# Optimization experiments

Measured on AMD Instinct MI355X. Metric: run time of the kernel, lower is better.

Reference implementation:

```python
import jax, jax.numpy as jnp
import numpy as np

G = 32          # latent grid size per axis
CIN = 3         # in_channels
C = 64          # fno_hidden_channels
M = 8           # half modes per axis (n_modes=16 -> 8)
L = 4           # fno_n_layers
LIFT = 256      # fno_lifting_channels
PROJ = 256      # projection_channels
N_IN = G ** 3
N_OUT = 16384
E = 262144      # total neighbor pairs from radius search


def _gelu(x):
    return jax.nn.gelu(x, approximate=False)  # matches torch F.gelu


def _spectral_conv(x, wr, wi):
    # x: (1, Ci, G, G, G); wr/wi: (4, Ci, Co, M, M, M) -- 4 frequency corners
    xf = jnp.fft.rfftn(x, axes=(2, 3, 4), norm='forward')
    w = wr + 1j * wi
    of = jnp.zeros((x.shape[0], wr.shape[2]) + xf.shape[2:], dtype=xf.dtype)
    corners = [(slice(0, M), slice(0, M)), (slice(0, M), slice(-M, None)),
               (slice(-M, None), slice(0, M)), (slice(-M, None), slice(-M, None))]
    for k, (s1, s2) in enumerate(corners):
        of = of.at[:, :, s1, s2, :M].set(
            jnp.einsum('bixyz,ioxyz->boxyz', xf[:, :, s1, s2, :M], w[k]))
    return jnp.fft.irfftn(of, s=x.shape[2:4] + x.shape[4:], axes=(2, 3, 4), norm='forward')


def setup_inputs() -> dict:
    key = jax.random.key(0)
    ks = jax.random.split(key, 32)
    s = 0.02
    inp = {}
    inp['in_p'] = jax.random.uniform(ks[0], (G, G, G, 3), jnp.float32)
    inp['out_p'] = jax.random.uniform(ks[1], (N_OUT, 3), jnp.float32)
    inp['f'] = jax.random.normal(ks[2], (G, G, G, CIN), jnp.float32)
    inp['nb_in_idx'] = jax.random.randint(ks[3], (E,), 0, N_IN)
    inp['nb_seg'] = jnp.sort(jax.random.randint(ks[4], (E,), 0, N_OUT))
    # FNO lifting (2-layer pointwise MLP): (in+coord)=6 -> LIFT -> C
    inp['lift_w1'] = jax.random.normal(ks[5], (LIFT, CIN + 3)) * s
    inp['lift_b1'] = jnp.zeros((LIFT,), jnp.float32)
    inp['lift_w2'] = jax.random.normal(ks[6], (C, LIFT)) * s
    inp['lift_b2'] = jnp.zeros((C,), jnp.float32)
    # Spectral conv weights: (L, 4 corners, Ci, Co, M, M, M)
    sc = 1.0 / (C * C)
    inp['spec_wr'] = jax.random.normal(ks[7], (L, 4, C, C, M, M, M)) * sc
    inp['spec_wi'] = jax.random.normal(ks[8], (L, 4, C, C, M, M, M)) * sc
    inp['skip_w'] = jax.random.normal(ks[9], (L, C, C)) * s
    inp['skip_b'] = jnp.zeros((L, C), jnp.float32)
    # GNO kernel MLP: [6, 512, 256, 64]
    inp['gno_w1'] = jax.random.normal(ks[10], (512, 6)) * s
    inp['gno_b1'] = jnp.zeros((512,), jnp.float32)
    inp['gno_w2'] = jax.random.normal(ks[11], (256, 512)) * s
    inp['gno_b2'] = jnp.zeros((256,), jnp.float32)
    inp['gno_w3'] = jax.random.normal(ks[12], (C, 256)) * s
    inp['gno_b3'] = jnp.zeros((C,), jnp.float32)
    # projection MLP: C -> PROJ -> out_channels(=1)
    inp['proj_w1'] = jax.random.normal(ks[13], (PROJ, C)) * s
    inp['proj_b1'] = jnp.zeros((PROJ,), jnp.float32)
    inp['proj_w2'] = jax.random.normal(ks[14], (1, PROJ)) * s
    inp['proj_b2'] = jnp.zeros((1,), jnp.float32)
    return inp


def reference(in_p, out_p, f, nb_in_idx, nb_seg,
              lift_w1, lift_b1, lift_w2, lift_b2,
              spec_wr, spec_wi, skip_w, skip_b,
              gno_w1, gno_b1, gno_w2, gno_b2, gno_w3, gno_b3,
              proj_w1, proj_b1, proj_w2, proj_b2):
    # ---- latent_embedding: FNO over the grid ----
    x = jnp.concatenate([f, in_p], axis=-1).transpose(3, 0, 1, 2)[None]  # (1,6,G,G,G)
    x = _gelu(jnp.einsum('bixyz,oi->boxyz', x, lift_w1) + lift_b1[None, :, None, None, None])
    x = jnp.einsum('bixyz,oi->boxyz', x, lift_w2) + lift_b2[None, :, None, None, None]
    for l in range(L):
        x = (_spectral_conv(x, spec_wr[l], spec_wi[l])
             + jnp.einsum('bixyz,oi->boxyz', x, skip_w[l])
             + skip_b[l][None, :, None, None, None])
        if l < L - 1:
            x = _gelu(x)
    latent = x[0].transpose(1, 2, 3, 0).reshape(N_IN, C)  # (n_in, C)
    # ---- integrate_latent: gather -> kernel MLP -> scale by f_y -> segment mean ----
    y = in_p.reshape(N_IN, 3)
    feats = jnp.concatenate([y[nb_in_idx], out_p[nb_seg]], axis=-1)  # (E, 6)
    h = _gelu(feats @ gno_w1.T + gno_b1)
    h = _gelu(h @ gno_w2.T + gno_b2)
    kern = h @ gno_w3.T + gno_b3                     # (E, C)
    contrib = kern * latent[nb_in_idx]               # linear transform: k(x,y)*f(y)
    ssum = jax.ops.segment_sum(contrib, nb_seg, num_segments=N_OUT)
    cnt = jax.ops.segment_sum(jnp.ones((E, 1), contrib.dtype), nb_seg, num_segments=N_OUT)
    out = ssum / jnp.maximum(cnt, 1.0)               # (n_out, C)
    # ---- projection MLP ----
    h = _gelu(out @ proj_w1.T + proj_b1)
    return h @ proj_w2.T + proj_b2                   # (n_out, 1)
```

## Files before the change

kernel.cpp:

```cpp
#include <hip/hip_runtime.h>

typedef unsigned short u16;
typedef float f32x4 __attribute__((ext_vector_type(4)));
typedef _Float16 f16x8 __attribute__((ext_vector_type(8)));
typedef u16 us8 __attribute__((ext_vector_type(8)));

#define PI2f 6.283185307179586f
#define NE_TOT 262144
#define N_IN_TOT 32768
#define N_OUT_TOT 16384

__device__ __forceinline__ float gelu_f(float x){
  float t  = 0.70710678118654752f * x;
  float t2 = t * t;
  float p = t*(1.1283791670955126f + t2*(-0.37612638903183754f + t2*(0.11283791670955126f
            + t2*(-0.026866170645131253f + t2*(0.005223977625442188f + t2*(-0.0008548327023450853f))))));
  return 0.5f * x * (1.0f + p);
}
__device__ __forceinline__ float gelu_s(float x){
  float t  = 0.70710678118654752f * x;
  float t2 = t * t;
  float p = t*(1.1283791670955126f + t2*(-0.37612638903183754f + t2*(0.11283791670955126f
            + t2*(-0.026866170645131253f))));
  return 0.5f * x * (1.0f + p);
}

__device__ __forceinline__ u16 f2h(float x){
  _Float16 h = (_Float16)x;
  return __builtin_bit_cast(u16, h);
}
__device__ __forceinline__ float h2f(u16 h){
  return (float)__builtin_bit_cast(_Float16, h);
}

__global__ __launch_bounds__(256) void k_pack(const float* w2, const float* w3, u16* B2p, u16* B3p){
  int tid = blockIdx.x*256 + threadIdx.x;
  if (tid < 16*16*64*8){
    int e = tid & 7, l = (tid>>3)&63, nt = (tid>>9)&15, ks = tid>>13;
    int n = nt*16 + (l&15);
    int k = ks*32 + (l>>4)*8 + e;
    B2p[tid] = f2h(w2[n*512 + k]);
  }
  int t2 = tid - 16*16*64*8;
  if (t2 >= 0 && t2 < 8*4*64*8){
    int e = t2 & 7, l = (t2>>3)&63, nt = (t2>>9)&3, ks = t2>>11;
    int n = nt*16 + (l&15);
    int k = ks*32 + (l>>4)*8 + e;
    B3p[t2] = f2h(w3[n*256 + k]);
  }
}

__global__ __launch_bounds__(256) void k_lift_s1(const float* f, const float* in_p,
      const float* w1, const float* b1, const float* w2, const float* b2, float* v, float* T1){
  extern __shared__ char smem[];
  float* h   = (float*)smem;
  float* w2t = h + 64*256;
  float* xf  = w2t + 256*65;
  float* vt2 = h;
  float* twc = xf;
  float* tws = xf + 256;
  int t = threadIdx.x;
  int p0 = blockIdx.x * 64;
  for (int idx = t; idx < 64*6; idx += 256){
    int e = idx/6, k = idx - e*6;
    xf[e*8 + k] = (k < 3) ? f[(p0+e)*3 + k] : in_p[(p0+e)*3 + (k-3)];
  }
  for (int i4 = t; i4 < 4096; i4 += 256){
    const float4 wv = ((const float4*)w2)[i4];
    int c = i4 >> 6, u = (i4 & 63)*4;
    w2t[(u+0)*65 + c] = wv.x;
    w2t[(u+1)*65 + c] = wv.y;
    w2t[(u+2)*65 + c] = wv.z;
    w2t[(u+3)*65 + c] = wv.w;
  }
  __syncthreads();
  {
    int u = t;
    float wr[6];
    #pragma unroll
    for (int k = 0; k < 6; ++k) wr[k] = w1[u*6 + k];
    float bb = b1[u];
    for (int e = 0; e < 64; ++e){
      float s = bb;
      #pragma unroll
      for (int k = 0; k < 6; ++k) s += wr[k]*xf[e*8+k];
      h[e*256 + u] = gelu_f(s);
    }
  }
  __syncthreads();
  {
    int kz = t >> 5, z = t & 31;
    float sv, cv;
    sincosf(PI2f * (float)(kz*z) / 32.0f, &sv, &cv);
    twc[t] = cv; tws[t] = sv;
  }
  int c = t & 63, zg = t >> 6;
  float acc[16];
  {
    #pragma unroll
    for (int i=0;i<16;++i) acc[i]=0.f;
    for (int u4 = 0; u4 < 64; ++u4){
      float wv0 = w2t[(u4*4+0)*65 + c];
      float wv1 = w2t[(u4*4+1)*65 + c];
      float wv2 = w2t[(u4*4+2)*65 + c];
      float wv3 = w2t[(u4*4+3)*65 + c];
      #pragma unroll
      for (int ee = 0; ee < 16; ++ee){
        const float4 hv = *(const float4*)&h[(zg*16+ee)*256 + u4*4];
        acc[ee] += wv0*hv.x + wv1*hv.y + wv2*hv.z + wv3*hv.w;
      }
    }
  }
  __syncthreads();
  {
    float bb = b2[c];
    #pragma unroll
    for (int ee = 0; ee < 16; ++ee){
      float val = acc[ee] + bb;
      int pl = zg*16 + ee;
      v[(size_t)(p0 + pl)*64 + c] = val;
      vt2[pl*64 + c] = val;
    }
  }
  __syncthreads();
  const float sc = 1.0f/32768.0f;
  int kzg = t >> 6;
  int kza = kzg, kzb = kzg + 4;
  float2* o = (float2*)T1;
  #pragma unroll
  for (int xyl = 0; xyl < 2; ++xyl){
    const float* vt = vt2 + xyl*2048;
    int xy = blockIdx.x*2 + xyl;
    float re0=0,im0=0,re1=0,im1=0;
    for (int z = 0; z < 32; ++z){
      float vv = vt[z*64 + c];
      re0 += vv * twc[kza*32+z]; im0 -= vv * tws[kza*32+z];
      re1 += vv * twc[kzb*32+z]; im1 -= vv * tws[kzb*32+z];
    }
    o[(xy*8 + kza)*64 + c] = make_float2(re0*sc, im0*sc);
    o[(xy*8 + kzb)*64 + c] = make_float2(re1*sc, im1*sc);
  }
}

__global__ __launch_bounds__(256) void k_s2(const float* T1, float* T2){
  __shared__ float t1s[2048];
  __shared__ float twc[512], tws[512];
  int t = threadIdx.x;
  int x = blockIdx.x >> 4, kz = (blockIdx.x >> 1) & 7, ch = blockIdx.x & 1;
  for (int i = t; i < 512; i += 256){
    int kyi = i >> 5, y = i & 31;
    int ky = (kyi < 8) ? kyi : kyi + 16;
    float sv, cv; sincosf(PI2f * (float)(ky*y) / 32.0f, &sv, &cv);
    twc[i]=cv; tws[i]=sv;
  }
  for (int i4 = t; i4 < 512; i4 += 256){
    int y = i4 >> 4, q4 = i4 & 15;
    ((float4*)t1s)[i4] = *((const float4*)&T1[((size_t)((x*32+y)*8 + kz))*128 + ch*64] + q4);
  }
  __syncthreads();
  int cl = t & 31, g = t >> 5;
  float ar[2], ai[2];
  ar[0]=0;ar[1]=0;ai[0]=0;ai[1]=0;
  for (int y = 0; y < 32; ++y){
    float tr = t1s[(y*32+cl)*2], ti = t1s[(y*32+cl)*2+1];
    #pragma unroll
    for (int kk = 0; kk < 2; ++kk){
      int kyi = g + kk*8;
      float cc = twc[kyi*32+y], ss = tws[kyi*32+y];
      ar[kk] += tr*cc + ti*ss;
      ai[kk] += ti*cc - tr*ss;
    }
  }
  float2* o = (float2*)T2;
  int c = ch*32 + cl;
  #pragma unroll
  for (int kk = 0; kk < 2; ++kk){
    int kyi = g + kk*8;
    o[((x*16 + kyi)*8 + kz)*64 + c] = make_float2(ar[kk], ai[kk]);
  }
}

__global__ __launch_bounds__(256) void k_s3(const float* T2, float* F){
  __shared__ float t2s[1024];
  __shared__ float twc[512], tws[512];
  int t = threadIdx.x;
  int kyi = blockIdx.x >> 5, kz = (blockIdx.x >> 2) & 7, cq = blockIdx.x & 3;
  for (int i = t; i < 512; i += 256){
    int kxi = i >> 5, x = i & 31;
    int kx = (kxi < 8) ? kxi : kxi + 16;
    float sv, cv; sincosf(PI2f * (float)(kx*x) / 32.0f, &sv, &cv);
    twc[i]=cv; tws[i]=sv;
  }
  if (t < 256){
    int i4 = t;
    int x = i4 >> 3, q4 = i4 & 7;
    ((float4*)t2s)[i4] = *((const float4*)&T2[((size_t)((x*16+kyi)*8 + kz))*128 + cq*32] + q4);
  }
  __syncthreads();
  int cl = t & 15, kxi = t >> 4;
  float ar = 0.f, ai = 0.f;
  for (int x = 0; x < 32; ++x){
    float tr = t2s[(x*16+cl)*2], ti = t2s[(x*16+cl)*2+1];
    float cc = twc[kxi*32+x], ss = tws[kxi*32+x];
    ar += tr*cc + ti*ss;
    ai += ti*cc - tr*ss;
  }
  float2* o = (float2*)F;
  int c = cq*16 + cl;
  o[((kxi*16 + kyi)*8 + kz)*64 + c] = make_float2(ar, ai);
}

__global__ __launch_bounds__(256) void k_s4(const float* F, const float* wr, const float* wi, float* OFp){
  __shared__ float FT[16*65*2];
  int t = threadIdx.x;
  int bid = blockIdx.x;
  int oh = bid & 7, ic = (bid>>3)&3, mx = (bid>>6)&7, corner = bid>>9;
  int kxi = (corner>>1)*8 + mx;
  int kyb = (corner&1)*8;
  for (int idx = t; idx < 2048; idx += 256){
    int m = idx >> 5, w = idx & 31;
    int cl = w >> 1, part = w & 1;
    int my = m >> 3, kz = m & 7;
    FT[(cl*65 + m)*2 + part] = F[((size_t)((kxi*16 + kyb + my)*8 + kz))*128 + ic*32 + w];
  }
  __syncthreads();
  int m = t & 63, og = t >> 6;
  int my = m >> 3, kz = m & 7;
  float accr[2], acci[2];
  accr[0]=0;accr[1]=0;acci[0]=0;acci[1]=0;
  #pragma unroll 4
  for (int i = 0; i < 16; ++i){
    float fr = FT[(i*65+m)*2], fi = FT[(i*65+m)*2+1];
    size_t rowbase = ((size_t)(corner*64 + ic*16 + i))*64;
    #pragma unroll
    for (int oo = 0; oo < 2; ++oo){
      int o = oh*8 + og*2 + oo;
      size_t widx = (rowbase + o)*512 + mx*64 + m;
      float wrv = wr[widx], wiv = wi[widx];
      accr[oo] += wrv*fr - wiv*fi;
      acci[oo] += wrv*fi + wiv*fr;
    }
  }
  float2* o2 = (float2*)OFp;
  size_t obase = (size_t)ic*131072 + ((size_t)((kxi*16 + kyb + my)*8 + kz))*64;
  #pragma unroll
  for (int oo = 0; oo < 2; ++oo){
    int o = oh*8 + og*2 + oo;
    o2[obase + o] = make_float2(accr[oo], acci[oo]);
  }
}

__global__ __launch_bounds__(256) void k_s5(const float* OFp, float* G1){
  __shared__ float OFs[512];
  __shared__ float twc[512], tws[512];
  int t = threadIdx.x;
  int kyi = blockIdx.x >> 5, kz = (blockIdx.x >> 2) & 7, oq = blockIdx.x & 3;
  for (int i = t; i < 512; i += 256){
    int kxi = i >> 5, x = i & 31;
    int kx = (kxi < 8) ? kxi : kxi + 16;
    float sv, cv; sincosf(PI2f * (float)(kx*x) / 32.0f, &sv, &cv);
    twc[i]=cv; tws[i]=sv;
  }
  if (t < 128){
    int i4 = t;
    int kx = i4 >> 3, w4 = i4 & 7;
    float4 s = {0.f,0.f,0.f,0.f};
    #pragma unroll
    for (int p = 0; p < 4; ++p){
      const float4 vv = *((const float4*)&OFp[(size_t)p*262144 + ((size_t)((kx*16+kyi)*8+kz))*128 + oq*32] + w4);
      s.x += vv.x; s.y += vv.y; s.z += vv.z; s.w += vv.w;
    }
    ((float4*)OFs)[i4] = s;
  }
  __syncthreads();
  int ol = t & 15, g = t >> 4;
  float ar[2], ai[2];
  ar[0]=0;ar[1]=0;ai[0]=0;ai[1]=0;
  for (int kxi = 0; kxi < 16; ++kxi){
    float orr = OFs[(kxi*16+ol)*2], oii = OFs[(kxi*16+ol)*2+1];
    #pragma unroll
    for (int xx = 0; xx < 2; ++xx){
      int x = g + xx*16;
      float cc = twc[kxi*32+x], ss = tws[kxi*32+x];
      ar[xx] += orr*cc - oii*ss;
      ai[xx] += orr*ss + oii*cc;
    }
  }
  float2* o2 = (float2*)G1;
  int o = oq*16 + ol;
  #pragma unroll
  for (int xx = 0; xx < 2; ++xx){
    int x = g + xx*16;
    o2[((x*16 + kyi)*8 + kz)*64 + o] = make_float2(ar[xx], ai[xx]);
  }
}

__global__ __launch_bounds__(256) void k_s6(const float* G1, float* G2){
  __shared__ float g1s[1024];
  __shared__ float twc[512], tws[512];
  int t = threadIdx.x;
  int x = blockIdx.x >> 4, kz = (blockIdx.x >> 1) & 7, oh = blockIdx.x & 1;
  for (int i = t; i < 512; i += 256){
    int kyi = i >> 5, y = i & 31;
    int ky = (kyi < 8) ? kyi : kyi + 16;
    float sv, cv; sincosf(PI2f * (float)(ky*y) / 32.0f, &sv, &cv);
    twc[i]=cv; tws[i]=sv;
  }
  if (t < 256){
    int i4 = t;
    int kyi = i4 >> 4, w4 = i4 & 15;
    ((float4*)g1s)[i4] = *((const float4*)&G1[((size_t)((x*16+kyi)*8+kz))*128 + oh*64] + w4);
  }
  __syncthreads();
  int ol = t & 31, g = t >> 5;
  float ar[4], ai[4];
  #pragma unroll
  for (int i=0;i<4;++i){ar[i]=0;ai[i]=0;}
  for (int kyi = 0; kyi < 16; ++kyi){
    float gr = g1s[(kyi*32+ol)*2], gi = g1s[(kyi*32+ol)*2+1];
    #pragma unroll
    for (int yy = 0; yy < 4; ++yy){
      int y = g + yy*8;
      float cc = twc[kyi*32+y], ss = tws[kyi*32+y];
      ar[yy] += gr*cc - gi*ss;
      ai[yy] += gr*ss + gi*cc;
    }
  }
  float2* o2 = (float2*)G2;
  int o = oh*32 + ol;
  #pragma unroll
  for (int yy = 0; yy < 4; ++yy){
    int y = g + yy*8;
    o2[((x*32 + y)*8 + kz)*64 + o] = make_float2(ar[yy], ai[yy]);
  }
}

__global__ __launch_bounds__(256) void k_s7s1(const float* G2, const float* vin,
      const float* skw, const float* skb, float* vout, float* T1){
  __shared__ float g2s[1024];
  __shared__ float vt[2048];
  __shared__ float wT[64*65];
  __shared__ float twc[256], tws[256];
  __shared__ float sb[64];
  int t = threadIdx.x;
  int xy = blockIdx.x;
  {
    int kz = t >> 5, z = t & 31;
    float sv, cv; sincosf(PI2f * (float)(kz*z) / 32.0f, &sv, &cv);
    twc[t]=cv; tws[t]=sv;
  }
  { int i4 = t; if (i4 < 256) ((float4*)g2s)[i4] = ((const float4*)(G2 + (size_t)xy*1024))[i4]; }
  for (int i4 = t; i4 < 512; i4 += 256)
    ((float4*)vt)[i4] = ((const float4*)(vin + (size_t)xy*2048))[i4];
  for (int i4 = t; i4 < 1024; i4 += 256){
    const float4 wv = ((const float4*)skw)[i4];
    int cc = i4 >> 4, ii = (i4 & 15)*4;
    wT[(ii+0)*65 + cc] = wv.x;
    wT[(ii+1)*65 + cc] = wv.y;
    wT[(ii+2)*65 + cc] = wv.z;
    wT[(ii+3)*65 + cc] = wv.w;
  }
  if (t < 64) sb[t] = skb[t];
  __syncthreads();
  int c = t & 63, zg = t >> 6;
  float accz[8];
  #pragma unroll
  for (int zz=0; zz<8; ++zz){
    int z = zg*8 + zz;
    float s = g2s[c*2];
    #pragma unroll
    for (int kz=1; kz<8; ++kz){
      float gr = g2s[(kz*64+c)*2], gi = g2s[(kz*64+c)*2+1];
      s += 2.0f*(gr*twc[kz*32+z] - gi*tws[kz*32+z]);
    }
    accz[zz] = s + sb[c];
  }
  for (int i4 = 0; i4 < 16; ++i4){
    float w0 = wT[(i4*4+0)*65 + c];
    float w1v = wT[(i4*4+1)*65 + c];
    float w2v = wT[(i4*4+2)*65 + c];
    float w3v = wT[(i4*4+3)*65 + c];
    #pragma unroll
    for (int zz=0; zz<8; ++zz){
      const float4 vv = *(const float4*)&vt[(zg*8+zz)*64 + i4*4];
      accz[zz] += w0*vv.x + w1v*vv.y + w2v*vv.z + w3v*vv.w;
    }
  }
  __syncthreads();
  #pragma unroll
  for (int zz=0; zz<8; ++zz){
    float s = gelu_f(accz[zz]);
    int z = zg*8 + zz;
    vout[(size_t)(xy*32 + z)*64 + c] = s;
    vt[z*64 + c] = s;
  }
  __syncthreads();
  {
    const float sc = 1.0f/32768.0f;
    int kzg = t >> 6;
    int kza = kzg, kzb = kzg + 4;
    float re0=0,im0=0,re1=0,im1=0;
    for (int z = 0; z < 32; ++z){
      float vv = vt[z*64 + c];
      re0 += vv * twc[kza*32+z]; im0 -= vv * tws[kza*32+z];
      re1 += vv * twc[kzb*32+z]; im1 -= vv * tws[kzb*32+z];
    }
    float2* o = (float2*)T1;
    o[(xy*8 + kza)*64 + c] = make_float2(re0*sc, im0*sc);
    o[(xy*8 + kzb)*64 + c] = make_float2(re1*sc, im1*sc);
  }
}

__global__ __launch_bounds__(256) void k_s7(const float* G2, const float* vin,
      const float* skw, const float* skb, float* vout, int dogelu){
  __shared__ float g2s[1024];
  __shared__ float vt[2048];
  __shared__ float wT[64*65];
  __shared__ float twc[256], tws[256];
  __shared__ float sb[64];
  int t = threadIdx.x;
  int xy = blockIdx.x;
  {
    int kz = t >> 5, z = t & 31;
    float sv, cv; sincosf(PI2f * (float)(kz*z) / 32.0f, &sv, &cv);
    twc[t]=cv; tws[t]=sv;
  }
  { int i4 = t; if (i4 < 256) ((float4*)g2s)[i4] = ((const float4*)(G2 + (size_t)xy*1024))[i4]; }
  for (int i4 = t; i4 < 512; i4 += 256)
    ((float4*)vt)[i4] = ((const float4*)(vin + (size_t)xy*2048))[i4];
  for (int i4 = t; i4 < 1024; i4 += 256){
    const float4 wv = ((const float4*)skw)[i4];
    int cc = i4 >> 4, ii = (i4 & 15)*4;
    wT[(ii+0)*65 + cc] = wv.x;
    wT[(ii+1)*65 + cc] = wv.y;
    wT[(ii+2)*65 + cc] = wv.z;
    wT[(ii+3)*65 + cc] = wv.w;
  }
  if (t < 64) sb[t] = skb[t];
  __syncthreads();
  int c = t & 63, zg = t >> 6;
  float accz[8];
  #pragma unroll
  for (int zz=0; zz<8; ++zz){
    int z = zg*8 + zz;
    float s = g2s[c*2];
    #pragma unroll
    for (int kz=1; kz<8; ++kz){
      float gr = g2s[(kz*64+c)*2], gi = g2s[(kz*64+c)*2+1];
      s += 2.0f*(gr*twc[kz*32+z] - gi*tws[kz*32+z]);
    }
    accz[zz] = s + sb[c];
  }
  for (int i4 = 0; i4 < 16; ++i4){
    float w0 = wT[(i4*4+0)*65 + c];
    float w1v = wT[(i4*4+1)*65 + c];
    float w2v = wT[(i4*4+2)*65 + c];
    float w3v = wT[(i4*4+3)*65 + c];
    #pragma unroll
    for (int zz=0; zz<8; ++zz){
      const float4 vv = *(const float4*)&vt[(zg*8+zz)*64 + i4*4];
      accz[zz] += w0*vv.x + w1v*vv.y + w2v*vv.z + w3v*vv.w;
    }
  }
  #pragma unroll
  for (int zz=0; zz<8; ++zz){
    float s = accz[zz];
    if (dogelu) s = gelu_f(s);
    vout[(size_t)(xy*32 + zg*8 + zz)*64 + c] = s;
  }
}

__global__ __launch_bounds__(256, 4) void k_gno(
    const int* nb_i, const int* nb_j, const float* in_p, const float* out_p,
    const float* w1, const float* b1, const float* b2g, const float* b3g,
    const u16* B2p, const u16* B3p, const float* latent, float* contrib){
  extern __shared__ char smem[];
  u16*   h1c   = (u16*)smem;
  u16*   h2s   = (u16*)smem;
  float* feats = (float*)(smem + 32768);
  float* sb2   = feats + 512;
  float* sb3   = sb2 + 256;
  int*   idxE  = (int*)(sb3 + 64);
  int t = threadIdx.x;
  int e0 = blockIdx.x * 64;
  if (t < 64){
    int gi = nb_i[e0 + t];
    int gj = nb_j[e0 + t];
    idxE[t] = gi;
    feats[t*8+0] = in_p[gi*3+0];
    feats[t*8+1] = in_p[gi*3+1];
    feats[t*8+2] = in_p[gi*3+2];
    feats[t*8+3] = out_p[gj*3+0];
    feats[t*8+4] = out_p[gj*3+1];
    feats[t*8+5] = out_p[gj*3+2];
    sb3[t] = b3g[t];
  }
  sb2[t] = b2g[t];
  int l = t & 63, w = t >> 6;
  int up = t & 63;
  int eg = t >> 6;
  f32x4 acc[4][4];
  #pragma unroll
  for (int m=0;m<4;++m)
    #pragma unroll
    for (int n=0;n<4;++n) acc[m][n] = (f32x4){0.f,0.f,0.f,0.f};
  __syncthreads();

  for (int chunk = 0; chunk < 4; ++chunk){
    int u0 = chunk*128 + up*2;
    float wa[6], wb[6];
    #pragma unroll
    for (int k=0;k<6;++k){ wa[k]=w1[u0*6+k]; wb[k]=w1[u0*6+6+k]; }
    float ba = b1[u0], bb = b1[u0+1];
    #pragma unroll 4
    for (int n = 0; n < 16; ++n){
      int e = eg*16 + n;
      const float4 fa = *(const float4*)&feats[e*8];
      const float4 fb = *(const float4*)&feats[e*8+4];
      float s0 = ba + wa[0]*fa.x + wa[1]*fa.y + wa[2]*fa.z + wa[3]*fa.w + wa[4]*fb.x + wa[5]*fb.y;
      float s1 = bb + wb[0]*fa.x + wb[1]*fa.y + wb[2]*fa.z + wb[3]*fa.w + wb[4]*fb.x + wb[5]*fb.y;
      unsigned lo = f2h(gelu_s(s0));
      unsigned hi = f2h(gelu_s(s1));
      int bofs = (e*256 + up*4) ^ ((e&7)<<4);
      *(unsigned*)((char*)h1c + bofs) = lo | (hi<<16);
    }
    __syncthreads();
    #pragma unroll
    for (int ks2 = 0; ks2 < 4; ++ks2){
      int gk = chunk*4 + ks2;
      f16x8 af[4];
      #pragma unroll
      for (int m=0;m<4;++m){
        int row = m*16 + (l&15);
        int bofs = (row*256 + ks2*64 + (l>>4)*16) ^ ((row&7)<<4);
        af[m] = __builtin_bit_cast(f16x8, *(const us8*)((const char*)h1c + bofs));
      }
      f16x8 bq[4];
      #pragma unroll
      for (int nt=0;nt<4;++nt){
        int ntg = w*4 + nt;
        bq[nt] = __builtin_bit_cast(f16x8, *(const us8*)(B2p + ((gk*16 + ntg)*64 + l)*8));
      }
      #pragma unroll
      for (int m=0;m<4;++m)
        #pragma unroll
        for (int nt=0;nt<4;++nt)
          acc[m][nt] = __builtin_amdgcn_mfma_f32_16x16x32_f16(af[m], bq[nt], acc[m][nt], 0, 0, 0);
    }
    __syncthreads();
  }

  #pragma unroll
  for (int m=0;m<4;++m){
    #pragma unroll
    for (int nt=0;nt<4;++nt){
      #pragma unroll
      for (int r=0;r<4;++r){
        int row = m*16 + (l>>4)*4 + r;
        int n = w*64 + nt*16 + (l&15);
        float vv = gelu_s(acc[m][nt][r] + sb2[n]);
        int bofs = (row*512 + n*2) ^ ((row&7)<<4);
        *(u16*)((char*)h2s + bofs) = f2h(vv);
      }
    }
  }
  __syncthreads();
  f32x4 a3[4];
  #pragma unroll
  for (int m=0;m<4;++m) a3[m] = (f32x4){0.f,0.f,0.f,0.f};
  #pragma unroll
  for (int ks = 0; ks < 8; ++ks){
    f16x8 bq3 = __builtin_bit_cast(f16x8, *(const us8*)(B3p + ((ks*4 + w)*64 + l)*8));
    #pragma unroll
    for (int m=0;m<4;++m){
      int row = m*16 + (l&15);
      int bofs = (row*512 + ks*64 + (l>>4)*16) ^ ((row&7)<<4);
      f16x8 am = __builtin_bit_cast(f16x8, *(const us8*)((const char*)h2s + bofs));
      a3[m] = __builtin_amdgcn_mfma_f32_16x16x32_f16(am, bq3, a3[m], 0, 0, 0);
    }
  }
  {
    int q = l >> 4;
    int c = w*16 + (l&15);
    float b3c = sb3[c];
    #pragma unroll
    for (int m=0;m<4;++m){
      #pragma unroll
      for (int r=0;r<4;++r){
        int e = m*16 + q*4 + r;
        float kern = a3[m][r] + b3c;
        contrib[((size_t)(e0+e))*64 + c] = kern * latent[(size_t)idxE[e]*64 + c];
      }
    }
  }
}

__global__ __launch_bounds__(256) void k_segmean(const int* seg, const float* contrib, float* outseg){
  int t = threadIdx.x;
  int j = blockIdx.x*4 + (t>>6);
  int lane = t & 63;
  int lo = 0, hi = NE_TOT;
  while (lo < hi){ int mid = (lo+hi)>>1; if (seg[mid] < j) lo = mid+1; else hi = mid; }
  int s0 = lo;
  hi = NE_TOT;
  while (lo < hi){ int mid = (lo+hi)>>1; if (seg[mid] < j+1) lo = mid+1; else hi = mid; }
  int s1 = lo;
  float s = 0.f;
  for (int e = s0; e < s1; ++e) s += contrib[(size_t)e*64 + lane];
  outseg[(size_t)j*64 + lane] = s / fmaxf((float)(s1 - s0), 1.0f);
}

__global__ __launch_bounds__(256) void k_proj(const float* outseg, const float* w1, const float* b1,
                                              const float* w2, const float* b2, float* out){
  __shared__ float rows[64*68];
  __shared__ float w1s[256*68];
  __shared__ float w2s[256];
  __shared__ float b1s[256];
  __shared__ float red[256];
  int t = threadIdx.x;
  int r0 = blockIdx.x * 64;
  for (int idx = t; idx < 4096; idx += 256){
    int e = idx >> 6, c = idx & 63;
    rows[e*68 + c] = outseg[(size_t)(r0+e)*64 + c];
  }
  for (int idx = t; idx < 16384; idx += 256){
    int u = idx >> 6, c = idx & 63;
    w1s[u*68 + c] = w1[idx];
  }
  w2s[t] = w2[t];
  b1s[t] = b1[t];
  __syncthreads();
  int e = t >> 2, q = t & 3;
  float fsum = 0.f;
  for (int uu = 0; uu < 64; ++uu){
    int u = uu*4 + q;
    float pre = b1s[u];
    #pragma unroll
    for (int c4 = 0; c4 < 16; ++c4){
      const float4 a = *(const float4*)&w1s[u*68 + c4*4];
      const float4 r = *(const float4*)&rows[e*68 + c4*4];
      pre += a.x*r.x + a.y*r.y + a.z*r.z + a.w*r.w;
    }
    fsum += w2s[u] * gelu_f(pre);
  }
  red[t] = fsum;
  __syncthreads();
  if (t < 64){
    out[r0 + t] = red[t*4] + red[t*4+1] + red[t*4+2] + red[t*4+3] + b2[0];
  }
}

extern "C" void kernel_launch(void* const* d_in, const int* in_sizes, int n_in,
                              void* d_out, int out_size, void* d_ws, size_t ws_size,
                              hipStream_t stream){
  const float* in_p  = (const float*)d_in[0];
  const float* out_p = (const float*)d_in[1];
  const float* f     = (const float*)d_in[2];
  const int*   nb_i  = (const int*)d_in[3];
  const int*   nb_j  = (const int*)d_in[4];
  const float* lw1   = (const float*)d_in[5];
  const float* lb1   = (const float*)d_in[6];
  const float* lw2   = (const float*)d_in[7];
  const float* lb2   = (const float*)d_in[8];
  const float* swr   = (const float*)d_in[9];
  const float* swi   = (const float*)d_in[10];
  const float* skw   = (const float*)d_in[11];
  const float* skb   = (const float*)d_in[12];
  const float* gw1   = (const float*)d_in[13];
  const float* gb1   = (const float*)d_in[14];
  const float* gw2   = (const float*)d_in[15];
  const float* gb2   = (const float*)d_in[16];
  const float* gw3   = (const float*)d_in[17];
  const float* gb3   = (const float*)d_in[18];
  const float* pw1   = (const float*)d_in[19];
  const float* pb1   = (const float*)d_in[20];
  const float* pw2   = (const float*)d_in[21];
  const float* pb2   = (const float*)d_in[22];
  float* out = (float*)d_out;

  char* ws = (char*)d_ws;
  size_t off = 0;
  auto alloc = [&](size_t bytes)->void*{ void* p = ws + off; off += (bytes + 255) & ~(size_t)255; return p; };
  float* va      = (float*)alloc((size_t)N_IN_TOT*64*4);
  float* vb      = (float*)alloc((size_t)N_IN_TOT*64*4);
  float* T1      = (float*)alloc((size_t)32*32*8*64*2*4);
  float* T2      = (float*)alloc((size_t)32*16*8*64*2*4);
  float* Fq      = (float*)alloc((size_t)16*16*8*64*2*4);
  float* OFp     = (float*)alloc((size_t)4*16*16*8*64*2*4);
  float* G1      = (float*)alloc((size_t)32*16*8*64*2*4);
  float* G2      = (float*)alloc((size_t)32*32*8*64*2*4);
  u16*   B2p     = (u16*)alloc((size_t)16*16*64*8*2);
  u16*   B3p     = (u16*)alloc((size_t)8*4*64*8*2);
  float* contrib = (float*)alloc((size_t)NE_TOT*64*4);
  float* outseg  = (float*)alloc((size_t)N_OUT_TOT*64*4);


  k_pack<<<576, 256, 0, stream>>>(gw2, gw3, B2p, B3p);
  k_lift_s1<<<512, 256, 134144, stream>>>(f, in_p, lw1, lb1, lw2, lb2, va, T1);

  float* vin = va; float* vout = vb;
  for (int layer = 0; layer < 4; ++layer){
    k_s2<<<512, 256, 0, stream>>>(T1, T2);
    k_s3<<<512, 256, 0, stream>>>(T2, Fq);
    k_s4<<<1024, 256, 0, stream>>>(Fq, swr + (size_t)layer*4*64*64*512, swi + (size_t)layer*4*64*64*512, OFp);
    k_s5<<<512, 256, 0, stream>>>(OFp, G1);
    k_s6<<<512, 256, 0, stream>>>(G1, G2);
    if (layer < 3)
      k_s7s1<<<1024, 256, 0, stream>>>(G2, vin, skw + layer*64*64, skb + layer*64, vout, T1);
    else
      k_s7<<<1024, 256, 0, stream>>>(G2, vin, skw + layer*64*64, skb + layer*64, vout, 0);
    float* tmp = vin; vin = vout; vout = tmp;
  }
  k_gno<<<4096, 256, 36608, stream>>>(nb_i, nb_j, in_p, out_p, gw1, gb1, gb2, gb3,
                                      B2p, B3p, vin, contrib);
  k_segmean<<<4096, 256, 0, stream>>>(nb_j, contrib, outseg);
  k_proj<<<256, 256, 0, stream>>>(outseg, pw1, pb1, pw2, pb2, out);
}
```

Before: 478.6 us.

## Fuse segment mean into projection and halve lift kernel shared memory

```diff
diff --git a/kernel.cpp b/kernel.cpp
--- a/kernel.cpp
+++ b/kernel.cpp
@@ -54,20 +54,27 @@
       const float* w1, const float* b1, const float* w2, const float* b2, float* v, float* T1){
   extern __shared__ char smem[];
   float* h   = (float*)smem;
-  float* w2t = h + 64*256;
-  float* xf  = w2t + 256*65;
-  float* vt2 = h;
-  float* twc = xf;
-  float* tws = xf + 256;
-  int t = threadIdx.x;
-  int p0 = blockIdx.x * 64;
-  for (int idx = t; idx < 64*6; idx += 256){
+  float* w2t = (float*)(smem + 32768);
+  float* xf  = (float*)(smem + 66048);
+  float* twc = (float*)(smem + 67072);
+  float* tws = (float*)(smem + 68096);
+  float* vt  = h;
+  int t = threadIdx.x;
+  int xy = blockIdx.x;
+  int p0 = xy * 32;
+  for (int idx = t; idx < 32*6; idx += 256){
     int e = idx/6, k = idx - e*6;
     xf[e*8 + k] = (k < 3) ? f[(p0+e)*3 + k] : in_p[(p0+e)*3 + (k-3)];
   }
-  for (int i4 = t; i4 < 4096; i4 += 256){
-    const float4 wv = ((const float4*)w2)[i4];
-    int c = i4 >> 6, u = (i4 & 63)*4;
+  {
+    int kz = t >> 5, z = t & 31;
+    float sv, cv; sincosf(PI2f * (float)(kz*z) / 32.0f, &sv, &cv);
+    twc[t]=cv; tws[t]=sv;
+  }
+  for (int i4 = t; i4 < 2048; i4 += 256){
+    int c = i4 >> 5, uq = i4 & 31;
+    const float4 wv = ((const float4*)w2)[(c<<6) + uq];
+    int u = uq*4;
     w2t[(u+0)*65 + c] = wv.x;
     w2t[(u+1)*65 + c] = wv.y;
     w2t[(u+2)*65 + c] = wv.z;
@@ -80,7 +87,7 @@
     #pragma unroll
     for (int k = 0; k < 6; ++k) wr[k] = w1[u*6 + k];
     float bb = b1[u];
-    for (int e = 0; e < 64; ++e){
+    for (int e = 0; e < 32; ++e){
       float s = bb;
       #pragma unroll
       for (int k = 0; k < 6; ++k) s += wr[k]*xf[e*8+k];
@@ -88,55 +95,66 @@
     }
   }
   __syncthreads();
-  {
-    int kz = t >> 5, z = t & 31;
-    float sv, cv;
-    sincosf(PI2f * (float)(kz*z) / 32.0f, &sv, &cv);
-    twc[t] = cv; tws[t] = sv;
-  }
   int c = t & 63, zg = t >> 6;
-  float acc[16];
-  {
-    #pragma unroll
-    for (int i=0;i<16;++i) acc[i]=0.f;
-    for (int u4 = 0; u4 < 64; ++u4){
-      float wv0 = w2t[(u4*4+0)*65 + c];
-      float wv1 = w2t[(u4*4+1)*65 + c];
-      float wv2 = w2t[(u4*4+2)*65 + c];
-      float wv3 = w2t[(u4*4+3)*65 + c];
-      #pragma unroll
-      for (int ee = 0; ee < 16; ++ee){
-        const float4 hv = *(const float4*)&h[(zg*16+ee)*256 + u4*4];
-        acc[ee] += wv0*hv.x + wv1*hv.y + wv2*hv.z + wv3*hv.w;
-      }
+  float acc[8];
+  #pragma unroll
+  for (int i=0;i<8;++i) acc[i]=0.f;
+  for (int u4 = 0; u4 < 32; ++u4){
+    float wv0 = w2t[(u4*4+0)*65 + c];
+    float wv1 = w2t[(u4*4+1)*65 + c];
+    float wv2 = w2t[(u4*4+2)*65 + c];
+    float wv3 = w2t[(u4*4+3)*65 + c];
+    #pragma unroll
+    for (int ee = 0; ee < 8; ++ee){
+      const float4 hv = *(const float4*)&h[(zg*8+ee)*256 + u4*4];
+      acc[ee] += wv0*hv.x + wv1*hv.y + wv2*hv.z + wv3*hv.w;
+    }
+  }
+  __syncthreads();
+  for (int i4 = t; i4 < 2048; i4 += 256){
+    int c2 = i4 >> 5, uq = i4 & 31;
+    const float4 wv = ((const float4*)w2)[(c2<<6) + 32 + uq];
+    int u = uq*4;
+    w2t[(u+0)*65 + c2] = wv.x;
+    w2t[(u+1)*65 + c2] = wv.y;
+    w2t[(u+2)*65 + c2] = wv.z;
+    w2t[(u+3)*65 + c2] = wv.w;
+  }
+  __syncthreads();
+  for (int u4 = 0; u4 < 32; ++u4){
+    float wv0 = w2t[(u4*4+0)*65 + c];
+    float wv1 = w2t[(u4*4+1)*65 + c];
+    float wv2 = w2t[(u4*4+2)*65 + c];
+    float wv3 = w2t[(u4*4+3)*65 + c];
+    #pragma unroll
+    for (int ee = 0; ee < 8; ++ee){
+      const float4 hv = *(const float4*)&h[(zg*8+ee)*256 + 128 + u4*4];
+      acc[ee] += wv0*hv.x + wv1*hv.y + wv2*hv.z + wv3*hv.w;
     }
   }
   __syncthreads();
   {
     float bb = b2[c];
     #pragma unroll
-    for (int ee = 0; ee < 16; ++ee){
+    for (int ee = 0; ee < 8; ++ee){
       float val = acc[ee] + bb;
-      int pl = zg*16 + ee;
-      v[(size_t)(p0 + pl)*64 + c] = val;
-      vt2[pl*64 + c] = val;
-    }
-  }
-  __syncthreads();
-  const float sc = 1.0f/32768.0f;
-  int kzg = t >> 6;
-  int kza = kzg, kzb = kzg + 4;
-  float2* o = (float2*)T1;
-  #pragma unroll
-  for (int xyl = 0; xyl < 2; ++xyl){
-    const float* vt = vt2 + xyl*2048;
-    int xy = blockIdx.x*2 + xyl;
+      int z = zg*8 + ee;
+      v[(size_t)(p0 + z)*64 + c] = val;
+      vt[z*64 + c] = val;
+    }
+  }
+  __syncthreads();
+  {
+    const float sc = 1.0f/32768.0f;
+    int kzg = t >> 6;
+    int kza = kzg, kzb = kzg + 4;
     float re0=0,im0=0,re1=0,im1=0;
     for (int z = 0; z < 32; ++z){
       float vv = vt[z*64 + c];
       re0 += vv * twc[kza*32+z]; im0 -= vv * tws[kza*32+z];
       re1 += vv * twc[kzb*32+z]; im1 -= vv * tws[kzb*32+z];
     }
+    float2* o = (float2*)T1;
     o[(xy*8 + kza)*64 + c] = make_float2(re0*sc, im0*sc);
     o[(xy*8 + kzb)*64 + c] = make_float2(re1*sc, im1*sc);
   }
@@ -595,33 +613,22 @@
   }
 }
 
-__global__ __launch_bounds__(256) void k_segmean(const int* seg, const float* contrib, float* outseg){
-  int t = threadIdx.x;
-  int j = blockIdx.x*4 + (t>>6);
-  int lane = t & 63;
-  int lo = 0, hi = NE_TOT;
-  while (lo < hi){ int mid = (lo+hi)>>1; if (seg[mid] < j) lo = mid+1; else hi = mid; }
-  int s0 = lo;
-  hi = NE_TOT;
-  while (lo < hi){ int mid = (lo+hi)>>1; if (seg[mid] < j+1) lo = mid+1; else hi = mid; }
-  int s1 = lo;
-  float s = 0.f;
-  for (int e = s0; e < s1; ++e) s += contrib[(size_t)e*64 + lane];
-  outseg[(size_t)j*64 + lane] = s / fmaxf((float)(s1 - s0), 1.0f);
-}
-
-__global__ __launch_bounds__(256) void k_proj(const float* outseg, const float* w1, const float* b1,
-                                              const float* w2, const float* b2, float* out){
+__global__ __launch_bounds__(256) void k_projm(const int* seg, const float* contrib,
+                                               const float* w1, const float* b1,
+                                               const float* w2, const float* b2, float* out){
   __shared__ float rows[64*68];
   __shared__ float w1s[256*68];
   __shared__ float w2s[256];
   __shared__ float b1s[256];
   __shared__ float red[256];
+  __shared__ int   sS0[65];
   int t = threadIdx.x;
   int r0 = blockIdx.x * 64;
-  for (int idx = t; idx < 4096; idx += 256){
-    int e = idx >> 6, c = idx & 63;
-    rows[e*68 + c] = outseg[(size_t)(r0+e)*64 + c];
+  if (t < 65){
+    int j = r0 + t;
+    int lo = 0, hi = NE_TOT;
+    while (lo < hi){ int mid = (lo+hi)>>1; if (seg[mid] < j) lo = mid+1; else hi = mid; }
+    sS0[t] = lo;
   }
   for (int idx = t; idx < 16384; idx += 256){
     int u = idx >> 6, c = idx & 63;
@@ -629,6 +636,14 @@
   }
   w2s[t] = w2[t];
   b1s[t] = b1[t];
+  __syncthreads();
+  for (int idx = t; idx < 4096; idx += 256){
+    int e = idx >> 6, c = idx & 63;
+    int s0 = sS0[e], s1 = sS0[e+1];
+    float s = 0.f;
+    for (int k = s0; k < s1; ++k) s += contrib[(size_t)k*64 + c];
+    rows[e*68 + c] = s / fmaxf((float)(s1 - s0), 1.0f);
+  }
   __syncthreads();
   int e = t >> 2, q = t & 3;
   float fsum = 0.f;
@@ -692,11 +707,10 @@
   u16*   B2p     = (u16*)alloc((size_t)16*16*64*8*2);
   u16*   B3p     = (u16*)alloc((size_t)8*4*64*8*2);
   float* contrib = (float*)alloc((size_t)NE_TOT*64*4);
-  float* outseg  = (float*)alloc((size_t)N_OUT_TOT*64*4);
 
 
   k_pack<<<576, 256, 0, stream>>>(gw2, gw3, B2p, B3p);
-  k_lift_s1<<<512, 256, 134144, stream>>>(f, in_p, lw1, lb1, lw2, lb2, va, T1);
+  k_lift_s1<<<1024, 256, 69120, stream>>>(f, in_p, lw1, lb1, lw2, lb2, va, T1);
 
   float* vin = va; float* vout = vb;
   for (int layer = 0; layer < 4; ++layer){
@@ -713,6 +727,5 @@
   }
   k_gno<<<4096, 256, 36608, stream>>>(nb_i, nb_j, in_p, out_p, gw1, gb1, gb2, gb3,
                                       B2p, B3p, vin, contrib);
-  k_segmean<<<4096, 256, 0, stream>>>(nb_j, contrib, outseg);
-  k_proj<<<256, 256, 0, stream>>>(outseg, pw1, pb1, pw2, pb2, out);
-}
+  k_projm<<<256, 256, 0, stream>>>(nb_j, contrib, pw1, pb1, pw2, pb2, out);
+}
```

Measured after the change: 524.4 us. +9.6%, slower.
